# Performance work log

Measured on AMD Instinct MI355X. Metric: run time of the kernel, lower is better.

The kernel has to match this reference:

```python
import jax, jax.numpy as jnp
import numpy as np

DIM, H, MAX_K, RADIUS, KNN_K, ALPHA, LN_EPS = 128, 4, 32, 0.3, 8, 2, 1e-5
DH = DIM // H
SCALE = DH ** -0.5


def _layernorm(x, w, b):
    mu = jnp.mean(x, axis=-1, keepdims=True)
    var = jnp.mean((x - mu) ** 2, axis=-1, keepdims=True)
    return (x - mu) * jax.lax.rsqrt(var + LN_EPS) * w + b


def setup_inputs() -> dict:
    key = jax.random.key(0)
    ks = jax.random.split(key, 12)
    N, M = 50000, 2500
    init = lambda k, shape: (jax.random.normal(k, shape, jnp.float32) * 0.02)
    return {
        "xyz": jax.random.normal(ks[0], (N, 3), jnp.float32),
        "feats": jax.random.normal(ks[1], (N, DIM), jnp.float32),
        "Wq": init(ks[2], (DIM, DIM)),
        "Wk": init(ks[3], (DIM, DIM)),
        "Wv": init(ks[4], (DIM, DIM)),
        "Wo": init(ks[5], (DIM, DIM)),
        "bo": jnp.zeros((DIM,), jnp.float32),
        "n1w": jnp.ones((DIM,), jnp.float32),
        "n1b": jnp.zeros((DIM,), jnp.float32),
        "n2w": jnp.ones((DIM,), jnp.float32),
        "n2b": jnp.zeros((DIM,), jnp.float32),
        "W1": init(ks[6], (DIM, 4 * DIM)),
        "b1": jnp.zeros((4 * DIM,), jnp.float32),
        "W2": init(ks[7], (4 * DIM, DIM)),
        "b2": jnp.zeros((DIM,), jnp.float32),
        "Wp": init(ks[8], (DIM, DIM)),
        "bp": jnp.zeros((DIM,), jnp.float32),
        "idx_center": jax.random.randint(ks[9], (M,), 0, N),
    }


def reference(xyz, feats, Wq, Wk, Wv, Wo, bo, n1w, n1b, n2w, n2b, W1, b1, W2, b2, Wp, bp, idx_center):
    M = idx_center.shape[0]
    center_xyz = xyz[idx_center]          # (M,3)
    center_feat = feats[idx_center]       # (M,C)

    # euclidean distance matrix (M,N) via |a|^2+|b|^2-2ab, safe sqrt (0-grad at 0 like torch.cdist)
    d2 = (jnp.sum(center_xyz ** 2, -1)[:, None] + jnp.sum(xyz ** 2, -1)[None, :]
          - 2.0 * center_xyz @ xyz.T)
    d2 = jnp.maximum(d2, 0.0)
    pos = d2 > 0
    dist = jnp.where(pos, jnp.sqrt(jnp.where(pos, d2, 1.0)), 0.0)  # (M,N)

    # ball query: mask + top-max_k smallest distances
    nbr_mask = dist < RADIUS
    nbr_mask = nbr_mask.at[jnp.arange(M), idx_center].set(True)
    dist_masked = jnp.where(nbr_mask, dist, jnp.inf)
    neg_d, nbr_idx = jax.lax.top_k(-dist_masked, MAX_K)   # (M,K)
    nbr_dist = -neg_d
    mask_valid = jnp.isfinite(nbr_dist)                    # (M,K)

    # gather neighbor feats, zero where invalid
    nbr_feats = jnp.where(mask_valid[..., None], feats[nbr_idx], 0.0)  # (M,K,C)

    # masked local attention per center (tiny heads)
    q = (center_feat @ Wq).reshape(M, H, DH)                       # (M,H,D)
    k = (nbr_feats @ Wk).reshape(M, MAX_K, H, DH).transpose(0, 2, 1, 3)  # (M,H,K,D)
    v = (nbr_feats @ Wv).reshape(M, MAX_K, H, DH).transpose(0, 2, 1, 3)
    attn = jnp.einsum('mhd,mhkd->mhk', q * SCALE, k)
    attn = jnp.where(mask_valid[:, None, :], attn, -1e9)
    attn = jax.nn.softmax(attn, axis=-1)
    out = jnp.einsum('mhk,mhkd->mhd', attn, v)
    # faithful to torch: transpose(1,2) before flatten -> (M, D, H) layout
    out = jnp.swapaxes(out, 1, 2).reshape(M, DIM)
    upd = out @ Wo + bo

    cf = center_feat + _layernorm(upd, n1w, n1b)
    ffn = jax.nn.relu(cf @ W1 + b1) @ W2 + b2
    cf = cf + _layernorm(ffn, n2w, n2b)

    # KNN inverse-distance-weighted upsample back to all N points
    neg_v, knn_idx = jax.lax.top_k(-dist.T, KNN_K)   # (N,k)
    knn_dist = -neg_v
    w = 1.0 / (knn_dist + 1e-6) ** ALPHA
    w = w / jnp.sum(w, axis=-1, keepdims=True)
    out_feats = jnp.einsum('nk,nkc->nc', w, cf[knn_idx])  # (N,C)
    out_feats = out_feats + jax.nn.relu(out_feats @ Wp + bp)
    return feats + out_feats
```

## Files before the change

kernel.cpp:

```cpp
#include <hip/hip_runtime.h>
#include <hip/hip_bf16.h>
#include <stdint.h>

#define DIM    128
#define KMAX   32
#define LN_EPS 1e-5f
#define ATT_SCALE 0.17677669529663687f
#define CAND   2048
#define WTOT   214400
#define PB     32
#define NSTR2  72
#define KSTR   132

typedef unsigned long long u64;
static __device__ __forceinline__ float bf2f(__hip_bfloat16 x) { return __bfloat162float(x); }

static __device__ __forceinline__ float norm32(float x, float y, float z) {
    return __fadd_rn(__fadd_rn(__fmul_rn(x, x), __fmul_rn(y, y)), __fmul_rn(z, z));
}
static __device__ __forceinline__ float d2_32(float cx, float cy, float cz, float cw,
                                              float px, float py, float pz, float pw) {
    float dot = __fmaf_rn(cz, pz, __fmaf_rn(cy, py, __fmul_rn(cx, px)));
    return __fsub_rn(__fadd_rn(cw, pw), __fmul_rn(2.0f, dot));
}
static __device__ __forceinline__ float d2_to_dist(float d2) {
    d2 = fmaxf(d2, 0.0f);
    return (d2 > 0.0f) ? __fsqrt_rn(d2) : 0.0f;
}
static __device__ __forceinline__ float dist32(float cx, float cy, float cz, float cw,
                                               float px, float py, float pz, float pw) {
    return d2_to_dist(d2_32(cx, cy, cz, cw, px, py, pz, pw));
}

static __device__ __forceinline__ float ldf(const void* p, int f32, size_t i) {
    return f32 ? ((const float*)p)[i] : bf2f(((const __hip_bfloat16*)p)[i]);
}
static __device__ __forceinline__ int ldidx(const void* p, int i64, int m) {
    return i64 ? ((const int*)p)[2 * m] : ((const int*)p)[m];
}

struct Ptrs { const void* p[18]; int sz[18]; };

__global__ void probe_dtypes(Ptrs P, int* __restrict__ fl) {
    int j = threadIdx.x;
    if (j >= 18) return;
    const void* x = P.p[j];
    int sz = P.sz[j];
    int flag = 0;
    if (j == 17) {
        const int* ip = (const int*)x;
        int odd_zero = 1, even_nz = 0;
        for (int k = 0; k < 8 && 2 * k + 1 < sz * 2; ++k) {
            if (ip[2 * k + 1] != 0) odd_zero = 0;
            if (ip[2 * k] != 0) even_nz = 1;
        }
        flag = (odd_zero && even_nz) ? 1 : 0;
    } else {
        const __hip_bfloat16* hp = (const __hip_bfloat16*)x;
        int n = sz < 256 ? sz : 256;
        for (int i = 0; i < n; ++i) {
            float w = bf2f(hp[i]);
            if (w != w || fabsf(w) > 1000.0f) { flag = 1; break; }
        }
        if ((j == 7 || j == 9) && bf2f(hp[0]) == 0.0f) flag = 1;
    }
    fl[j] = flag;
}

__global__ __launch_bounds__(256) void conv_prep(Ptrs P, const int* __restrict__ fl,
                                                 float* __restrict__ Wf,
                                                 float4* __restrict__ pnt4,
                                                 float4* __restrict__ cent4,
                                                 int N, int M, int convB) {
    int b = blockIdx.x;
    if (b < convB) {
        int i = b * 256 + threadIdx.x;
        if (i >= WTOT) return;
        int j, off;
        if      (i < 16384)  { j = 2;  off = i; }
        else if (i < 32768)  { j = 3;  off = i - 16384; }
        else if (i < 49152)  { j = 4;  off = i - 32768; }
        else if (i < 65536)  { j = 5;  off = i - 49152; }
        else if (i < 131072) { j = 11; off = i - 65536; }
        else if (i < 196608) { j = 13; off = i - 131072; }
        else if (i < 212992) { j = 15; off = i - 196608; }
        else if (i < 213120) { j = 6;  off = i - 212992; }
        else if (i < 213248) { j = 7;  off = i - 213120; }
        else if (i < 213376) { j = 8;  off = i - 213248; }
        else if (i < 213504) { j = 9;  off = i - 213376; }
        else if (i < 213632) { j = 10; off = i - 213504; }
        else if (i < 214144) { j = 12; off = i - 213632; }
        else if (i < 214272) { j = 14; off = i - 214144; }
        else                 { j = 16; off = i - 214272; }
        Wf[i] = ldf(P.p[j], fl[j], off);
    } else {
        int i = (b - convB) * 256 + threadIdx.x;
        int f0 = fl[0];
        if (i < N) {
            float x = ldf(P.p[0], f0, 3 * i + 0);
            float y = ldf(P.p[0], f0, 3 * i + 1);
            float z = ldf(P.p[0], f0, 3 * i + 2);
            pnt4[i] = make_float4(x, y, z, norm32(x, y, z));
        }
        if (i < M) {
            int c = ldidx(P.p[17], fl[17], i);
            c = (c >= 0 && c < N) ? c : 0;
            float x = ldf(P.p[0], f0, 3 * c + 0);
            float y = ldf(P.p[0], f0, 3 * c + 1);
            float z = ldf(P.p[0], f0, 3 * c + 2);
            cent4[i] = make_float4(x, y, z, norm32(x, y, z));
        }
    }
}

__global__ __launch_bounds__(256) void ball_scan(
    const float4* __restrict__ pnt4,
    const float4* __restrict__ cent4,
    int N, int M, int* __restrict__ nbr_g) {

    __shared__ u64 key[2][CAND];
    __shared__ int s_cnt[2], s_ni[2][KMAX];

    int tid = threadIdx.x;
    int m0 = blockIdx.x * 2, m1 = m0 + 1;
    bool has1 = (m1 < M);
    float4 c0 = cent4[m0];
    float4 c1 = has1 ? cent4[m1] : make_float4(1e30f, 1e30f, 1e30f, 1e30f);

    if (tid < 2) s_cnt[tid] = 0;
    if (tid < KMAX) { s_ni[0][tid] = -1; s_ni[1][tid] = -1; }
    __syncthreads();

    for (int i = tid; i < N; i += 256) {
        float4 p = pnt4[i];
        float d20 = d2_32(c0.x, c0.y, c0.z, c0.w, p.x, p.y, p.z, p.w);
        if (d20 < 0.0901f) {
            float dist = d2_to_dist(d20);
            if (dist < 0.3f) {
                int pos = atomicAdd(&s_cnt[0], 1);
                if (pos < CAND)
                    key[0][pos] = ((u64)__float_as_uint(dist) << 32) | (unsigned)i;
            }
        }
        float d21 = d2_32(c1.x, c1.y, c1.z, c1.w, p.x, p.y, p.z, p.w);
        if (d21 < 0.0901f) {
            float dist = d2_to_dist(d21);
            if (dist < 0.3f) {
                int pos = atomicAdd(&s_cnt[1], 1);
                if (pos < CAND)
                    key[1][pos] = ((u64)__float_as_uint(dist) << 32) | (unsigned)i;
            }
        }
    }
    __syncthreads();

    int half = tid >> 7, t2 = tid & 127;
    int cnth = min(s_cnt[half], CAND);
    if (half == 1 && !has1) cnth = 0;
    for (int i = t2; i < cnth; i += 128) {
        u64 ki = key[half][i];
        int r = 0;
        for (int j = 0; j < cnth; ++j) r += (key[half][j] < ki) ? 1 : 0;
        if (r < KMAX) s_ni[half][r] = (int)(unsigned)(ki & 0xFFFFFFFFULL);
    }
    __syncthreads();
    if (tid < KMAX) nbr_g[m0 * KMAX + tid] = s_ni[0][tid];
    if (has1 && tid >= 128 && tid < 128 + KMAX)
        nbr_g[m1 * KMAX + (tid - 128)] = s_ni[1][tid - 128];
}

#define NFT2(cc, kk) R[(cc) * NSTR2 + (kk)]
#define SKV2(kk, col) R[(kk) * KSTR + (col)]

__global__ __launch_bounds__(256, 4) void attn_ffn(
    const int* __restrict__ nbr_g,
    const void* __restrict__ feats,
    const void* __restrict__ idxc,
    const int* __restrict__ fl,
    const float* __restrict__ Wf,
    float* __restrict__ cf_out, int N, int M) {

    const float* Wqf = Wf;
    const float* Wkf = Wf + 16384;
    const float* Wvf = Wf + 32768;
    const float* Wof = Wf + 49152;
    const float* W1f = Wf + 65536;
    const float* W2f = Wf + 131072;
    const float* Pf  = Wf + 212992;

    __shared__ __align__(16) float R[128 * NSTR2];
    __shared__ int   s_ni[2 * KMAX];
    __shared__ __align__(16) float s_cf[256], s_x[256];
    __shared__ float s_red[8];

    int tid = threadIdx.x;
    int lane = tid & 63, wv = tid >> 6;
    int center = tid >> 7, col = tid & 127;
    int m0 = blockIdx.x * 2;
    int f1 = fl[1], fi = fl[17];

    if (tid < 64) {
        int m2 = m0 + (tid >> 5);
        s_ni[tid] = (m2 < M) ? nbr_g[m2 * KMAX + (tid & 31)] : -1;
    }
    {
        int m2 = m0 + center; m2 = (m2 < M) ? m2 : (M - 1);
        int c = ldidx(idxc, fi, m2);
        c = (c >= 0 && c < N) ? c : 0;
        s_cf[tid] = ldf(feats, f1, (size_t)c * DIM + col);
    }
    __syncthreads();
    for (int t = tid; t < 64 * DIM; t += 256) {
        int kk2 = t >> 7, cc = t & 127;
        int idx = s_ni[kk2];
        float v = (idx >= 0 && idx < N) ? ldf(feats, f1, (size_t)idx * DIM + cc) : 0.0f;
        NFT2(cc, kk2) = v;
    }
    __syncthreads();

    int kq = tid >> 5, cq = tid & 31;
    int k0 = kq * 8, c0 = cq * 4;
    float ka[8][4], va[8][4];
#pragma unroll
    for (int j = 0; j < 8; ++j)
#pragma unroll
        for (int cc2 = 0; cc2 < 4; ++cc2) { ka[j][cc2] = 0.0f; va[j][cc2] = 0.0f; }

#pragma unroll 2
    for (int i = 0; i < DIM; ++i) {
        float4 n0  = *(const float4*)&NFT2(i, k0);
        float4 n1  = *(const float4*)&NFT2(i, k0 + 4);
        float4 wk  = *(const float4*)&Wkf[i * DIM + c0];
        float4 wv4 = *(const float4*)&Wvf[i * DIM + c0];
        float nn[8] = {n0.x, n0.y, n0.z, n0.w, n1.x, n1.y, n1.z, n1.w};
#pragma unroll
        for (int j = 0; j < 8; ++j) {
            float nj = nn[j];
            ka[j][0] = fmaf(nj, wk.x, ka[j][0]);
            ka[j][1] = fmaf(nj, wk.y, ka[j][1]);
            ka[j][2] = fmaf(nj, wk.z, ka[j][2]);
            ka[j][3] = fmaf(nj, wk.w, ka[j][3]);
            va[j][0] = fmaf(nj, wv4.x, va[j][0]);
            va[j][1] = fmaf(nj, wv4.y, va[j][1]);
            va[j][2] = fmaf(nj, wv4.z, va[j][2]);
            va[j][3] = fmaf(nj, wv4.w, va[j][3]);
        }
    }
    __syncthreads();

    float* s_q    = R + 8448;
    float* s_attn = R + 8704;
    float* s_ao   = R + 8960;

#pragma unroll
    for (int j = 0; j < 8; ++j)
        *(float4*)&SKV2(k0 + j, c0) = make_float4(ka[j][0], ka[j][1], ka[j][2], ka[j][3]);
    {
        float acc = 0.0f;
        const float* cfc = s_cf + center * 128;
#pragma unroll 4
        for (int i = 0; i < DIM; i += 4) {
            float4 a = *(const float4*)&cfc[i];
            acc = fmaf(a.x, Wqf[(i + 0) * DIM + col], acc);
            acc = fmaf(a.y, Wqf[(i + 1) * DIM + col], acc);
            acc = fmaf(a.z, Wqf[(i + 2) * DIM + col], acc);
            acc = fmaf(a.w, Wqf[(i + 3) * DIM + col], acc);
        }
        s_q[tid] = acc;
    }
    __syncthreads();

    {
        int h = (tid >> 5) & 3, kk = tid & 31;
        float s = 0.0f;
#pragma unroll
        for (int d = 0; d < 32; ++d)
            s = fmaf(s_q[center * 128 + h * 32 + d], SKV2(center * 32 + kk, h * 32 + d), s);
        s *= ATT_SCALE;
        if (s_ni[center * 32 + kk] < 0) s = -1e9f;
        float mx = s;
        for (int off = 16; off; off >>= 1) mx = fmaxf(mx, __shfl_xor(mx, off, 32));
        float e = expf(s - mx);
        float sm = e;
        for (int off = 16; off; off >>= 1) sm += __shfl_xor(sm, off, 32);
        sm = (sm > 0.0f) ? sm : 1.0f;
        s_attn[tid] = e / sm;
    }
    __syncthreads();
#pragma unroll
    for (int j = 0; j < 8; ++j)
        *(float4*)&SKV2(k0 + j, c0) = make_float4(va[j][0], va[j][1], va[j][2], va[j][3]);
    __syncthreads();

    {
        int h = (tid >> 5) & 3, d = tid & 31;
        float o = 0.0f;
#pragma unroll
        for (int kk = 0; kk < KMAX; ++kk)
            o = fmaf(s_attn[center * 128 + h * 32 + kk], SKV2(center * 32 + kk, h * 32 + d), o);
        s_ao[center * 128 + d * 4 + h] = o;
    }
    __syncthreads();

    float upd = Pf[0 + col];
    {
#pragma unroll 4
        for (int i = 0; i < DIM; i += 4) {
            float4 a = *(const float4*)&s_ao[center * 128 + i];
            upd = fmaf(a.x, Wof[(i + 0) * DIM + col], upd);
            upd = fmaf(a.y, Wof[(i + 1) * DIM + col], upd);
            upd = fmaf(a.z, Wof[(i + 2) * DIM + col], upd);
            upd = fmaf(a.w, Wof[(i + 3) * DIM + col], upd);
        }
        float sum = upd;
        for (int off = 32; off; off >>= 1) sum += __shfl_xor(sum, off, 64);
        if (lane == 0) s_red[wv] = sum;
    }
    __syncthreads();
    float mu = (s_red[center * 2] + s_red[center * 2 + 1]) * (1.0f / 128.0f);
    float xc = upd - mu;
    {
        float q2 = xc * xc;
        for (int off = 32; off; off >>= 1) q2 += __shfl_xor(q2, off, 64);
        if (lane == 0) s_red[4 + wv] = q2;
    }
    __syncthreads();
    float var = (s_red[4 + center * 2] + s_red[5 + center * 2]) * (1.0f / 128.0f);
    float cf1;
    {
        float rs = 1.0f / sqrtf(var + LN_EPS);
        float ln1 = fmaf(xc * rs, Pf[128 + col], Pf[256 + col]);
        cf1 = s_cf[tid] + ln1;
        s_x[tid] = cf1;
    }
    __syncthreads();

    float* s_h = R;
#pragma unroll
    for (int jj = 0; jj < 4; ++jj) {
        int j = col + 128 * jj;
        float a = Pf[640 + j];
#pragma unroll 4
        for (int i = 0; i < DIM; i += 4) {
            float4 v = *(const float4*)&s_x[center * 128 + i];
            a = fmaf(v.x, W1f[(i + 0) * 512 + j], a);
            a = fmaf(v.y, W1f[(i + 1) * 512 + j], a);
            a = fmaf(v.z, W1f[(i + 2) * 512 + j], a);
            a = fmaf(v.w, W1f[(i + 3) * 512 + j], a);
        }
        s_h[center * 512 + j] = fmaxf(a, 0.0f);
    }
    __syncthreads();

    float fa = Pf[1152 + col];
    {
        const float* hc = s_h + center * 512;
#pragma unroll 4
        for (int i = 0; i < 256; i += 4) {
            float4 v = *(const float4*)&hc[i];
            fa = fmaf(v.x, W2f[(i + 0) * DIM + col], fa);
            fa = fmaf(v.y, W2f[(i + 1) * DIM + col], fa);
            fa = fmaf(v.z, W2f[(i + 2) * DIM + col], fa);
            fa = fmaf(v.w, W2f[(i + 3) * DIM + col], fa);
        }
    }
    float fb = 0.0f;
    {
        const float* hc = s_h + center * 512;
#pragma unroll 4
        for (int i = 256; i < 512; i += 4) {
            float4 v = *(const float4*)&hc[i];
            fb = fmaf(v.x, W2f[(i + 0) * DIM + col], fb);
            fb = fmaf(v.y, W2f[(i + 1) * DIM + col], fb);
            fb = fmaf(v.z, W2f[(i + 2) * DIM + col], fb);
            fb = fmaf(v.w, W2f[(i + 3) * DIM + col], fb);
        }
    }
    float ffn = fa + fb;
    {
        float sum = ffn;
        for (int off = 32; off; off >>= 1) sum += __shfl_xor(sum, off, 64);
        if (lane == 0) s_red[wv] = sum;
    }
    __syncthreads();
    mu = (s_red[center * 2] + s_red[center * 2 + 1]) * (1.0f / 128.0f);
    xc = ffn - mu;
    {
        float q2 = xc * xc;
        for (int off = 32; off; off >>= 1) q2 += __shfl_xor(q2, off, 64);
        if (lane == 0) s_red[4 + wv] = q2;
    }
    __syncthreads();
    var = (s_red[4 + center * 2] + s_red[5 + center * 2]) * (1.0f / 128.0f);
    {
        float rs2 = 1.0f / sqrtf(var + LN_EPS);
        float ln2 = fmaf(xc * rs2, Pf[384 + col], Pf[512 + col]);
        int m2 = m0 + center;
        if (m2 < M) cf_out[(size_t)m2 * DIM + col] = cf1 + ln2;
    }
}

#define CSWAP(a, b) { if ((b) < (a)) { u64 t_ = (a); (a) = (b); (b) = t_; } }

static __device__ __forceinline__ float bound8(float vmn) {
    float v = vmn;
    v = fminf(v, __shfl_xor(v, 1, 64));
    v = fminf(v, __shfl_xor(v, 2, 64));
    v = fminf(v, __shfl_xor(v, 4, 64));
    v = fmaxf(v, __shfl_xor(v, 8, 64));
    v = fmaxf(v, __shfl_xor(v, 16, 64));
    v = fmaxf(v, __shfl_xor(v, 32, 64));
    return fmaxf(v, 0.0f) * 1.0000019073486328f;
}

__global__ __launch_bounds__(256) void knn_select(
    const float4* __restrict__ pnt4,
    const float4* __restrict__ cent4,
    const float* __restrict__ cf,
    float* __restrict__ upg,
    int N, int M) {

    __shared__ u64 s_buf[4][4][64];
    __shared__ u64 s_srt[4][4][8];
    __shared__ int s_cnt[4][4];

    int tid = threadIdx.x;
    int lane = tid & 63, wv = tid >> 6;
    int p0 = blockIdx.x * 16 + wv * 4;

    float4 pp[4];
    bool own[4];
#pragma unroll
    for (int e = 0; e < 4; ++e) {
        int p = p0 + e;
        own[e] = (p < N);
        pp[e] = own[e] ? pnt4[p] : make_float4(0.f, 0.f, 0.f, 0.f);
    }

    if (lane < 4) s_cnt[wv][lane] = 0;
    __syncthreads();

    float vmn[4] = {3.4e38f, 3.4e38f, 3.4e38f, 3.4e38f};
    for (int j = lane; j < M; j += 64) {
        float4 cc = cent4[j];
#pragma unroll
        for (int e = 0; e < 4; ++e)
            vmn[e] = fminf(vmn[e], d2_32(cc.x, cc.y, cc.z, cc.w,
                                         pp[e].x, pp[e].y, pp[e].z, pp[e].w));
    }
    float T[4];
#pragma unroll
    for (int e = 0; e < 4; ++e) T[e] = bound8(vmn[e]);

    for (int j = lane; j < M; j += 64) {
        float4 cc = cent4[j];
#pragma unroll
        for (int e = 0; e < 4; ++e) {
            float d2 = d2_32(cc.x, cc.y, cc.z, cc.w,
                             pp[e].x, pp[e].y, pp[e].z, pp[e].w);
            if (d2 <= T[e]) {
                float dist = d2_to_dist(d2);
                u64 key = ((u64)__float_as_uint(dist) << 32) | (unsigned)j;
                int pos = atomicAdd(&s_cnt[wv][e], 1);
                if (pos < 64) s_buf[wv][e][pos] = key;
            }
        }
    }

    int c0 = lane, c1 = lane + 64;
#pragma unroll
    for (int e = 0; e < 4; ++e) {
        int cnt = s_cnt[wv][e];
        if (cnt <= 64 && M >= 8) {
            u64 myk = (lane < cnt) ? s_buf[wv][e][lane] : ~0ULL;
            int r = 0;
            for (int i = 0; i < cnt; ++i) {
                u64 o = s_buf[wv][e][i];
                r += (o < myk) ? 1 : 0;
            }
            if (lane < cnt && r < 8) s_srt[wv][e][r] = myk;
        } else {
            float4 pq = pp[e];
            u64 f0 = ~0ULL, f1_ = ~0ULL, f2_ = ~0ULL, f3 = ~0ULL,
                f4 = ~0ULL, f5 = ~0ULL, f6 = ~0ULL, f7 = ~0ULL;
            for (int j = lane; j < M; j += 64) {
                float4 cc = cent4[j];
                float dist = dist32(cc.x, cc.y, cc.z, cc.w, pq.x, pq.y, pq.z, pq.w);
                u64 key = ((u64)__float_as_uint(dist) << 32) | (unsigned)j;
                if (key < f7) {
                    f7 = key;
                    CSWAP(f6, f7); CSWAP(f5, f6); CSWAP(f4, f5); CSWAP(f3, f4);
                    CSWAP(f2_, f3); CSWAP(f1_, f2_); CSWAP(f0, f1_);
                }
            }
            int ptr2 = 0;
            u64 cur2 = f0;
#pragma unroll
            for (int e2 = 0; e2 < 8; ++e2) {
                u64 v = cur2;
                for (int off = 32; off; off >>= 1) {
                    u64 o = __shfl_down(v, off, 64);
                    v = (o < v) ? o : v;
                }
                u64 gm = __shfl(v, 0, 64);
                if (lane == 0) s_srt[wv][e][e2] = gm;
                if (cur2 == gm) {
                    ptr2++;
                    cur2 = (ptr2 == 1) ? f1_ : (ptr2 == 2) ? f2_ : (ptr2 == 3) ? f3 :
                           (ptr2 == 4) ? f4 : (ptr2 == 5) ? f5 : (ptr2 == 6) ? f6 :
                           (ptr2 == 7) ? f7 : ~0ULL;
                }
            }
        }
        int   ki[8];
        float w8[8];
        float ws = 0.0f;
#pragma unroll
        for (int e2 = 0; e2 < 8; ++e2) {
            u64 gm = s_srt[wv][e][e2];
            float d = __uint_as_float((unsigned)(gm >> 32));
            int ci = (int)(unsigned)(gm & 0xFFFFFFFFULL);
            ci = (ci >= 0 && ci < M) ? ci : 0;
            float t = __fadd_rn(d, 1e-6f);
            float w = 1.0f / __fmul_rn(t, t);
            ws += w;
            ki[e2] = ci;
            w8[e2] = w;
        }
        float inv = 1.0f / ws;
#pragma unroll
        for (int k = 0; k < 8; ++k) w8[k] *= inv;

        float u0 = 0.0f, u1 = 0.0f;
#pragma unroll
        for (int k = 0; k < 8; ++k) {
            const float* row = cf + (size_t)ki[k] * DIM;
            u0 = fmaf(w8[k], row[c0], u0);
            u1 = fmaf(w8[k], row[c1], u1);
        }
        if (own[e]) {
            upg[(size_t)(p0 + e) * DIM + c0] = u0;
            upg[(size_t)(p0 + e) * DIM + c1] = u1;
        }
    }
}

__global__ __launch_bounds__(256) void wp_out(
    const float* __restrict__ Wf,
    const void* __restrict__ feats,
    const int* __restrict__ fl,
    float* __restrict__ out,
    int N) {

    const float* Wpf = Wf + 196608;
    const float* bpf = Wf + 212992 + 1280;

    __shared__ __align__(16) float s_up[PB][132];

    int tid = threadIdx.x;
    int p0 = blockIdx.x * PB;

    for (int f = tid; f < PB * 32; f += 256) {
        int p = f >> 5, i4 = (f & 31) << 2;
        float4 v = make_float4(0.f, 0.f, 0.f, 0.f);
        if (p0 + p < N) v = *(const float4*)&out[(size_t)(p0 + p) * DIM + i4];
        *(float4*)&s_up[p][i4] = v;
    }
    __syncthreads();

    int cq = tid & 31, pq = tid >> 5;
    int c0 = cq << 2;
    int pA = pq << 2;

    float a00 = 0.f, a01 = 0.f, a02 = 0.f, a03 = 0.f;
    float a10 = 0.f, a11 = 0.f, a12 = 0.f, a13 = 0.f;
    float a20 = 0.f, a21 = 0.f, a22 = 0.f, a23 = 0.f;
    float a30 = 0.f, a31 = 0.f, a32 = 0.f, a33 = 0.f;

#pragma unroll 4
    for (int i = 0; i < DIM; ++i) {
        float4 w = *(const float4*)&Wpf[(size_t)i * DIM + c0];
        float u0 = s_up[pA + 0][i];
        float u1 = s_up[pA + 1][i];
        float u2 = s_up[pA + 2][i];
        float u3 = s_up[pA + 3][i];
        a00 = fmaf(u0, w.x, a00); a01 = fmaf(u0, w.y, a01);
        a02 = fmaf(u0, w.z, a02); a03 = fmaf(u0, w.w, a03);
        a10 = fmaf(u1, w.x, a10); a11 = fmaf(u1, w.y, a11);
        a12 = fmaf(u1, w.z, a12); a13 = fmaf(u1, w.w, a13);
        a20 = fmaf(u2, w.x, a20); a21 = fmaf(u2, w.y, a21);
        a22 = fmaf(u2, w.z, a22); a23 = fmaf(u2, w.w, a23);
        a30 = fmaf(u3, w.x, a30); a31 = fmaf(u3, w.y, a31);
        a32 = fmaf(u3, w.z, a32); a33 = fmaf(u3, w.w, a33);
    }

    int f1v = fl[1];
    float4 bp4 = make_float4(bpf[c0 + 0], bpf[c0 + 1], bpf[c0 + 2], bpf[c0 + 3]);

    float accs[4][4] = {{a00, a01, a02, a03}, {a10, a11, a12, a13},
                        {a20, a21, a22, a23}, {a30, a31, a32, a33}};
#pragma unroll
    for (int a = 0; a < 4; ++a) {
        int p = p0 + pA + a;
        if (p < N) {
            float4 u = *(const float4*)&s_up[pA + a][c0];
            float4 o;
            o.x = ldf(feats, f1v, (size_t)p * DIM + c0 + 0) + u.x + fmaxf(bp4.x + accs[a][0], 0.0f);
            o.y = ldf(feats, f1v, (size_t)p * DIM + c0 + 1) + u.y + fmaxf(bp4.y + accs[a][1], 0.0f);
            o.z = ldf(feats, f1v, (size_t)p * DIM + c0 + 2) + u.z + fmaxf(bp4.z + accs[a][2], 0.0f);
            o.w = ldf(feats, f1v, (size_t)p * DIM + c0 + 3) + u.w + fmaxf(bp4.w + accs[a][3], 0.0f);
            *(float4*)&out[(size_t)p * DIM + c0] = o;
        }
    }
}

extern "C" void kernel_launch(void* const* d_in, const int* in_sizes, int n_in,
                              void* d_out, int out_size, void* d_ws, size_t ws_size,
                              hipStream_t stream) {
    int N = in_sizes[0] / 3;
    int M = in_sizes[17];

    Ptrs P;
    for (int j = 0; j < 18; ++j) { P.p[j] = d_in[j]; P.sz[j] = in_sizes[j]; }

    size_t off = 0;
    auto alloc = [&](size_t bytes) -> void* {
        off = (off + 255) & ~(size_t)255;
        void* p = (void*)((char*)d_ws + off);
        off += bytes;
        return p;
    };
    int*    fl    = (int*)alloc(32 * 4);
    float*  Wf    = (float*)alloc((size_t)WTOT * 4);
    float4* pnt4  = (float4*)alloc((size_t)N * 16);
    float4* cent4 = (float4*)alloc((size_t)M * 16);
    float*  cfbuf = (float*)alloc((size_t)M * DIM * 4);
    int*    nbr   = (int*)alloc((size_t)M * KMAX * 4);

    int convB = (WTOT + 255) / 256;
    int NM = (N > M) ? N : M;
    int prepB = (NM + 255) / 256;

    probe_dtypes<<<1, 32, 0, stream>>>(P, fl);
    conv_prep<<<convB + prepB, 256, 0, stream>>>(P, fl, Wf, pnt4, cent4, N, M, convB);
    ball_scan<<<(M + 1) / 2, 256, 0, stream>>>(pnt4, cent4, N, M, nbr);
    attn_ffn<<<(M + 1) / 2, 256, 0, stream>>>(nbr, d_in[1], d_in[17], fl, Wf, cfbuf, N, M);
    knn_select<<<(N + 15) / 16, 256, 0, stream>>>(pnt4, cent4, cfbuf, (float*)d_out, N, M);
    wp_out<<<(N + PB - 1) / PB, 256, 0, stream>>>(Wf, d_in[1], fl, (float*)d_out, N);
}
```

Before: 524.9 us.

## Split attention and FFN into separate kernels with register-resident K/V

The fused attention+FFN kernel is split in two. attn_core runs 512 threads, gathers neighbour features in two 64-channel chunks to cut shared memory, and keeps K/V in registers, computing QK with shuffles and PV with partial sums. It writes only cf1. A new ffn_ln kernel processes four centers per block, so each W1/W2 load is reused across several centers, then applies LN2. This trades an extra launch and a global round-trip of cf for more occupancy and better weight reuse.

```diff
diff --git a/kernel.cpp b/kernel.cpp
--- a/kernel.cpp
+++ b/kernel.cpp
@@ -9,8 +9,8 @@
 #define CAND   2048
 #define WTOT   214400
 #define PB     32
-#define NSTR2  72
-#define KSTR   132
+#define CH     64
+#define GSTR   68
 
 typedef unsigned long long u64;
 static __device__ __forceinline__ float bf2f(__hip_bfloat16 x) { return __bfloat162float(x); }
@@ -169,10 +169,7 @@
         nbr_g[m1 * KMAX + (tid - 128)] = s_ni[1][tid - 128];
 }
 
-#define NFT2(cc, kk) R[(cc) * NSTR2 + (kk)]
-#define SKV2(kk, col) R[(kk) * KSTR + (col)]
-
-__global__ __launch_bounds__(256, 4) void attn_ffn(
+__global__ __launch_bounds__(512, 6) void attn_core(
     const int* __restrict__ nbr_g,
     const void* __restrict__ feats,
     const void* __restrict__ idxc,
@@ -184,18 +181,16 @@
     const float* Wkf = Wf + 16384;
     const float* Wvf = Wf + 32768;
     const float* Wof = Wf + 49152;
-    const float* W1f = Wf + 65536;
-    const float* W2f = Wf + 131072;
     const float* Pf  = Wf + 212992;
 
-    __shared__ __align__(16) float R[128 * NSTR2];
+    __shared__ __align__(16) float G[CH * GSTR];
+    __shared__ __align__(16) float s_pv[16][128];
     __shared__ int   s_ni[2 * KMAX];
-    __shared__ __align__(16) float s_cf[256], s_x[256];
+    __shared__ __align__(16) float s_cf[256], s_q[256], s_attn[256], s_ao[256];
     __shared__ float s_red[8];
 
     int tid = threadIdx.x;
     int lane = tid & 63, wv = tid >> 6;
-    int center = tid >> 7, col = tid & 127;
     int m0 = blockIdx.x * 2;
     int f1 = fl[1], fi = fl[17];
 
@@ -203,59 +198,17 @@
         int m2 = m0 + (tid >> 5);
         s_ni[tid] = (m2 < M) ? nbr_g[m2 * KMAX + (tid & 31)] : -1;
     }
-    {
+    if (tid < 256) {
+        int center = tid >> 7, col = tid & 127;
         int m2 = m0 + center; m2 = (m2 < M) ? m2 : (M - 1);
         int c = ldidx(idxc, fi, m2);
         c = (c >= 0 && c < N) ? c : 0;
         s_cf[tid] = ldf(feats, f1, (size_t)c * DIM + col);
     }
     __syncthreads();
-    for (int t = tid; t < 64 * DIM; t += 256) {
-        int kk2 = t >> 7, cc = t & 127;
-        int idx = s_ni[kk2];
-        float v = (idx >= 0 && idx < N) ? ldf(feats, f1, (size_t)idx * DIM + cc) : 0.0f;
-        NFT2(cc, kk2) = v;
-    }
-    __syncthreads();
-
-    int kq = tid >> 5, cq = tid & 31;
-    int k0 = kq * 8, c0 = cq * 4;
-    float ka[8][4], va[8][4];
-#pragma unroll
-    for (int j = 0; j < 8; ++j)
-#pragma unroll
-        for (int cc2 = 0; cc2 < 4; ++cc2) { ka[j][cc2] = 0.0f; va[j][cc2] = 0.0f; }
-
-#pragma unroll 2
-    for (int i = 0; i < DIM; ++i) {
-        float4 n0  = *(const float4*)&NFT2(i, k0);
-        float4 n1  = *(const float4*)&NFT2(i, k0 + 4);
-        float4 wk  = *(const float4*)&Wkf[i * DIM + c0];
-        float4 wv4 = *(const float4*)&Wvf[i * DIM + c0];
-        float nn[8] = {n0.x, n0.y, n0.z, n0.w, n1.x, n1.y, n1.z, n1.w};
-#pragma unroll
-        for (int j = 0; j < 8; ++j) {
-            float nj = nn[j];
-            ka[j][0] = fmaf(nj, wk.x, ka[j][0]);
-            ka[j][1] = fmaf(nj, wk.y, ka[j][1]);
-            ka[j][2] = fmaf(nj, wk.z, ka[j][2]);
-            ka[j][3] = fmaf(nj, wk.w, ka[j][3]);
-            va[j][0] = fmaf(nj, wv4.x, va[j][0]);
-            va[j][1] = fmaf(nj, wv4.y, va[j][1]);
-            va[j][2] = fmaf(nj, wv4.z, va[j][2]);
-            va[j][3] = fmaf(nj, wv4.w, va[j][3]);
-        }
-    }
-    __syncthreads();
-
-    float* s_q    = R + 8448;
-    float* s_attn = R + 8704;
-    float* s_ao   = R + 8960;
-
-#pragma unroll
-    for (int j = 0; j < 8; ++j)
-        *(float4*)&SKV2(k0 + j, c0) = make_float4(ka[j][0], ka[j][1], ka[j][2], ka[j][3]);
-    {
+
+    if (tid < 256) {
+        int center = tid >> 7, col = tid & 127;
         float acc = 0.0f;
         const float* cfc = s_cf + center * 128;
 #pragma unroll 4
@@ -268,15 +221,77 @@
         }
         s_q[tid] = acc;
     }
-    __syncthreads();
+
+    int kq = tid >> 5;
+    int cq = tid & 31;
+    int k0 = kq * 4, c0 = cq * 4;
+    int cent = kq >> 3;
+    float ka[4][4], va[4][4];
+#pragma unroll
+    for (int j = 0; j < 4; ++j)
+#pragma unroll
+        for (int t = 0; t < 4; ++t) { ka[j][t] = 0.0f; va[j][t] = 0.0f; }
+
+    for (int r = 0; r < 2; ++r) {
+        if (r) __syncthreads();
+        for (int t = tid; t < 64 * CH; t += 512) {
+            int kk = t >> 6, cc = t & 63;
+            int idx = s_ni[kk];
+            float v = (idx >= 0 && idx < N)
+                    ? ldf(feats, f1, (size_t)idx * DIM + r * CH + cc) : 0.0f;
+            G[cc * GSTR + kk] = v;
+        }
+        __syncthreads();
+#pragma unroll 2
+        for (int i = 0; i < CH; ++i) {
+            float4 n = *(const float4*)&G[i * GSTR + k0];
+            int gi = r * CH + i;
+            float4 wk  = *(const float4*)&Wkf[gi * DIM + c0];
+            float4 wv4 = *(const float4*)&Wvf[gi * DIM + c0];
+            float nn[4] = {n.x, n.y, n.z, n.w};
+#pragma unroll
+            for (int j = 0; j < 4; ++j) {
+                float nj = nn[j];
+                ka[j][0] = fmaf(nj, wk.x, ka[j][0]);
+                ka[j][1] = fmaf(nj, wk.y, ka[j][1]);
+                ka[j][2] = fmaf(nj, wk.z, ka[j][2]);
+                ka[j][3] = fmaf(nj, wk.w, ka[j][3]);
+                va[j][0] = fmaf(nj, wv4.x, va[j][0]);
+                va[j][1] = fmaf(nj, wv4.y, va[j][1]);
+                va[j][2] = fmaf(nj, wv4.z, va[j][2]);
+                va[j][3] = fmaf(nj, wv4.w, va[j][3]);
+            }
+        }
+    }
 
     {
-        int h = (tid >> 5) & 3, kk = tid & 31;
-        float s = 0.0f;
-#pragma unroll
-        for (int d = 0; d < 32; ++d)
-            s = fmaf(s_q[center * 128 + h * 32 + d], SKV2(center * 32 + kk, h * 32 + d), s);
-        s *= ATT_SCALE;
+        const float* qc = s_q + cent * 128;
+        float part[4];
+#pragma unroll
+        for (int j = 0; j < 4; ++j) {
+            float p = 0.0f;
+            p = fmaf(qc[c0 + 0], ka[j][0], p);
+            p = fmaf(qc[c0 + 1], ka[j][1], p);
+            p = fmaf(qc[c0 + 2], ka[j][2], p);
+            p = fmaf(qc[c0 + 3], ka[j][3], p);
+            p += __shfl_xor(p, 1, 64);
+            p += __shfl_xor(p, 2, 64);
+            p += __shfl_xor(p, 4, 64);
+            part[j] = p;
+        }
+        if ((cq & 7) == 0) {
+            int h = cq >> 3;
+#pragma unroll
+            for (int j = 0; j < 4; ++j)
+                s_attn[cent * 128 + h * 32 + (kq & 7) * 4 + j] = part[j];
+        }
+    }
+    __syncthreads();
+
+    if (tid < 256) {
+        int center = tid >> 7;
+        int kk = tid & 31;
+        float s = s_attn[tid] * ATT_SCALE;
         if (s_ni[center * 32 + kk] < 0) s = -1e9f;
         float mx = s;
         for (int off = 16; off; off >>= 1) mx = fmaxf(mx, __shfl_xor(mx, off, 32));
@@ -287,23 +302,40 @@
         s_attn[tid] = e / sm;
     }
     __syncthreads();
-#pragma unroll
-    for (int j = 0; j < 8; ++j)
-        *(float4*)&SKV2(k0 + j, c0) = make_float4(va[j][0], va[j][1], va[j][2], va[j][3]);
-    __syncthreads();
 
     {
-        int h = (tid >> 5) & 3, d = tid & 31;
-        float o = 0.0f;
-#pragma unroll
-        for (int kk = 0; kk < KMAX; ++kk)
-            o = fmaf(s_attn[center * 128 + h * 32 + kk], SKV2(center * 32 + kk, h * 32 + d), o);
-        s_ao[center * 128 + d * 4 + h] = o;
-    }
-    __syncthreads();
-
-    float upd = Pf[0 + col];
-    {
+        int h = cq >> 3;
+        float pvp0 = 0.0f, pvp1 = 0.0f, pvp2 = 0.0f, pvp3 = 0.0f;
+#pragma unroll
+        for (int j = 0; j < 4; ++j) {
+            float a = s_attn[cent * 128 + h * 32 + (kq & 7) * 4 + j];
+            pvp0 = fmaf(a, va[j][0], pvp0);
+            pvp1 = fmaf(a, va[j][1], pvp1);
+            pvp2 = fmaf(a, va[j][2], pvp2);
+            pvp3 = fmaf(a, va[j][3], pvp3);
+        }
+        *(float4*)&s_pv[kq][c0] = make_float4(pvp0, pvp1, pvp2, pvp3);
+    }
+    __syncthreads();
+
+    if (tid < 256) {
+        int cb = tid >> 7, cc2 = tid & 127;
+        float o = s_pv[cb * 8 + 0][cc2];
+        o += s_pv[cb * 8 + 1][cc2];
+        o += s_pv[cb * 8 + 2][cc2];
+        o += s_pv[cb * 8 + 3][cc2];
+        o += s_pv[cb * 8 + 4][cc2];
+        o += s_pv[cb * 8 + 5][cc2];
+        o += s_pv[cb * 8 + 6][cc2];
+        o += s_pv[cb * 8 + 7][cc2];
+        s_ao[cb * 128 + (cc2 & 31) * 4 + (cc2 >> 5)] = o;
+    }
+    __syncthreads();
+
+    float upd = 0.0f, xc = 0.0f;
+    int center = tid >> 7, col = tid & 127;
+    if (tid < 256) {
+        upd = Pf[0 + col];
 #pragma unroll 4
         for (int i = 0; i < DIM; i += 4) {
             float4 a = *(const float4*)&s_ao[center * 128 + i];
@@ -317,86 +349,128 @@
         if (lane == 0) s_red[wv] = sum;
     }
     __syncthreads();
-    float mu = (s_red[center * 2] + s_red[center * 2 + 1]) * (1.0f / 128.0f);
-    float xc = upd - mu;
-    {
+    if (tid < 256) {
+        float mu = (s_red[center * 2] + s_red[center * 2 + 1]) * (1.0f / 128.0f);
+        xc = upd - mu;
         float q2 = xc * xc;
         for (int off = 32; off; off >>= 1) q2 += __shfl_xor(q2, off, 64);
         if (lane == 0) s_red[4 + wv] = q2;
     }
     __syncthreads();
-    float var = (s_red[4 + center * 2] + s_red[5 + center * 2]) * (1.0f / 128.0f);
-    float cf1;
-    {
+    if (tid < 256) {
+        float var = (s_red[4 + center * 2] + s_red[5 + center * 2]) * (1.0f / 128.0f);
         float rs = 1.0f / sqrtf(var + LN_EPS);
         float ln1 = fmaf(xc * rs, Pf[128 + col], Pf[256 + col]);
-        cf1 = s_cf[tid] + ln1;
-        s_x[tid] = cf1;
-    }
-    __syncthreads();
-
-    float* s_h = R;
-#pragma unroll
-    for (int jj = 0; jj < 4; ++jj) {
-        int j = col + 128 * jj;
-        float a = Pf[640 + j];
-#pragma unroll 4
-        for (int i = 0; i < DIM; i += 4) {
-            float4 v = *(const float4*)&s_x[center * 128 + i];
-            a = fmaf(v.x, W1f[(i + 0) * 512 + j], a);
-            a = fmaf(v.y, W1f[(i + 1) * 512 + j], a);
-            a = fmaf(v.z, W1f[(i + 2) * 512 + j], a);
-            a = fmaf(v.w, W1f[(i + 3) * 512 + j], a);
-        }
-        s_h[center * 512 + j] = fmaxf(a, 0.0f);
-    }
-    __syncthreads();
-
-    float fa = Pf[1152 + col];
+        float cf1 = s_cf[tid] + ln1;
+        int m2 = m0 + center;
+        if (m2 < M) cf_out[(size_t)m2 * DIM + col] = cf1;
+    }
+}
+
+__global__ __launch_bounds__(256) void ffn_ln(
+    const float* __restrict__ Wf,
+    float* __restrict__ cf, int M) {
+
+    const float* W1f = Wf + 65536;
+    const float* W2f = Wf + 131072;
+    const float* Pf  = Wf + 212992;
+
+    __shared__ __align__(16) float s_x[512];
+    __shared__ __align__(16) float s_h[2048];
+    __shared__ float s_p2[2][4][128];
+    __shared__ float s_red[8];
+
+    int tid = threadIdx.x, lane = tid & 63, wv = tid >> 6;
+    int m0 = blockIdx.x * 4;
+
+    for (int t = tid; t < 512; t += 256) {
+        int cent = t >> 7, c = t & 127;
+        int m = m0 + cent;
+        s_x[t] = (m < M) ? cf[(size_t)m * DIM + c] : 0.0f;
+    }
+    __syncthreads();
+
     {
-        const float* hc = s_h + center * 512;
-#pragma unroll 4
-        for (int i = 0; i < 256; i += 4) {
-            float4 v = *(const float4*)&hc[i];
-            fa = fmaf(v.x, W2f[(i + 0) * DIM + col], fa);
-            fa = fmaf(v.y, W2f[(i + 1) * DIM + col], fa);
-            fa = fmaf(v.z, W2f[(i + 2) * DIM + col], fa);
-            fa = fmaf(v.w, W2f[(i + 3) * DIM + col], fa);
-        }
-    }
-    float fb = 0.0f;
+        int pairh = tid >> 7;
+        int j0 = (tid & 127) * 4;
+        float4 b1q = *(const float4*)&Pf[640 + j0];
+        float aA0 = b1q.x, aA1 = b1q.y, aA2 = b1q.z, aA3 = b1q.w;
+        float aB0 = b1q.x, aB1 = b1q.y, aB2 = b1q.z, aB3 = b1q.w;
+        const float* xA = s_x + (2 * pairh) * 128;
+        const float* xB = s_x + (2 * pairh + 1) * 128;
+#pragma unroll 2
+        for (int i4 = 0; i4 < 32; ++i4) {
+            float4 xa = *(const float4*)&xA[i4 * 4];
+            float4 xb = *(const float4*)&xB[i4 * 4];
+#pragma unroll
+            for (int s = 0; s < 4; ++s) {
+                float4 w = *(const float4*)&W1f[(i4 * 4 + s) * 512 + j0];
+                float va_ = (&xa.x)[s], vb_ = (&xb.x)[s];
+                aA0 = fmaf(va_, w.x, aA0); aA1 = fmaf(va_, w.y, aA1);
+                aA2 = fmaf(va_, w.z, aA2); aA3 = fmaf(va_, w.w, aA3);
+                aB0 = fmaf(vb_, w.x, aB0); aB1 = fmaf(vb_, w.y, aB1);
+                aB2 = fmaf(vb_, w.z, aB2); aB3 = fmaf(vb_, w.w, aB3);
+            }
+        }
+        *(float4*)&s_h[(2 * pairh) * 512 + j0] =
+            make_float4(fmaxf(aA0, 0.0f), fmaxf(aA1, 0.0f), fmaxf(aA2, 0.0f), fmaxf(aA3, 0.0f));
+        *(float4*)&s_h[(2 * pairh + 1) * 512 + j0] =
+            make_float4(fmaxf(aB0, 0.0f), fmaxf(aB1, 0.0f), fmaxf(aB2, 0.0f), fmaxf(aB3, 0.0f));
+    }
+    __syncthreads();
+
     {
-        const float* hc = s_h + center * 512;
-#pragma unroll 4
-        for (int i = 256; i < 512; i += 4) {
-            float4 v = *(const float4*)&hc[i];
-            fb = fmaf(v.x, W2f[(i + 0) * DIM + col], fb);
-            fb = fmaf(v.y, W2f[(i + 1) * DIM + col], fb);
-            fb = fmaf(v.z, W2f[(i + 2) * DIM + col], fb);
-            fb = fmaf(v.w, W2f[(i + 3) * DIM + col], fb);
-        }
-    }
-    float ffn = fa + fb;
-    {
+        int kh = tid >> 7;
+        int c = tid & 127;
+        float acc0 = (kh == 0) ? Pf[1152 + c] : 0.0f;
+        float acc1 = acc0, acc2 = acc0, acc3 = acc0;
+        const float* h0 = s_h + 0 * 512 + kh * 256;
+        const float* h1 = s_h + 1 * 512 + kh * 256;
+        const float* h2 = s_h + 2 * 512 + kh * 256;
+        const float* h3 = s_h + 3 * 512 + kh * 256;
+#pragma unroll 2
+        for (int i4 = 0; i4 < 64; ++i4) {
+            float4 q0 = *(const float4*)&h0[i4 * 4];
+            float4 q1 = *(const float4*)&h1[i4 * 4];
+            float4 q2 = *(const float4*)&h2[i4 * 4];
+            float4 q3 = *(const float4*)&h3[i4 * 4];
+#pragma unroll
+            for (int s = 0; s < 4; ++s) {
+                float w = W2f[(kh * 256 + i4 * 4 + s) * DIM + c];
+                acc0 = fmaf((&q0.x)[s], w, acc0);
+                acc1 = fmaf((&q1.x)[s], w, acc1);
+                acc2 = fmaf((&q2.x)[s], w, acc2);
+                acc3 = fmaf((&q3.x)[s], w, acc3);
+            }
+        }
+        s_p2[kh][0][c] = acc0;
+        s_p2[kh][1][c] = acc1;
+        s_p2[kh][2][c] = acc2;
+        s_p2[kh][3][c] = acc3;
+    }
+    __syncthreads();
+
+    for (int rr = 0; rr < 2; ++rr) {
+        int cl = tid >> 7;
+        int cent = rr * 2 + cl;
+        int c = tid & 127;
+        float ffn = s_p2[0][cent][c] + s_p2[1][cent][c];
         float sum = ffn;
         for (int off = 32; off; off >>= 1) sum += __shfl_xor(sum, off, 64);
         if (lane == 0) s_red[wv] = sum;
-    }
-    __syncthreads();
-    mu = (s_red[center * 2] + s_red[center * 2 + 1]) * (1.0f / 128.0f);
-    xc = ffn - mu;
-    {
+        __syncthreads();
+        float mu = (s_red[cl * 2] + s_red[cl * 2 + 1]) * (1.0f / 128.0f);
+        float xc = ffn - mu;
         float q2 = xc * xc;
         for (int off = 32; off; off >>= 1) q2 += __shfl_xor(q2, off, 64);
         if (lane == 0) s_red[4 + wv] = q2;
-    }
-    __syncthreads();
-    var = (s_red[4 + center * 2] + s_red[5 + center * 2]) * (1.0f / 128.0f);
-    {
+        __syncthreads();
+        float var = (s_red[4 + cl * 2] + s_red[5 + cl * 2]) * (1.0f / 128.0f);
         float rs2 = 1.0f / sqrtf(var + LN_EPS);
-        float ln2 = fmaf(xc * rs2, Pf[384 + col], Pf[512 + col]);
-        int m2 = m0 + center;
-        if (m2 < M) cf_out[(size_t)m2 * DIM + col] = cf1 + ln2;
+        float ln2 = fmaf(xc * rs2, Pf[384 + c], Pf[512 + c]);
+        int m = m0 + cent;
+        if (m < M) cf[(size_t)m * DIM + c] = s_x[cent * 128 + c] + ln2;
+        __syncthreads();
     }
 }
 
@@ -644,7 +718,8 @@
     probe_dtypes<<<1, 32, 0, stream>>>(P, fl);
     conv_prep<<<convB + prepB, 256, 0, stream>>>(P, fl, Wf, pnt4, cent4, N, M, convB);
     ball_scan<<<(M + 1) / 2, 256, 0, stream>>>(pnt4, cent4, N, M, nbr);
-    attn_ffn<<<(M + 1) / 2, 256, 0, stream>>>(nbr, d_in[1], d_in[17], fl, Wf, cfbuf, N, M);
+    attn_core<<<(M + 1) / 2, 512, 0, stream>>>(nbr, d_in[1], d_in[17], fl, Wf, cfbuf, N, M);
+    ffn_ln<<<(M + 3) / 4, 256, 0, stream>>>(Wf, cfbuf, M);
     knn_select<<<(N + 15) / 16, 256, 0, stream>>>(pnt4, cent4, cfbuf, (float*)d_out, N, M);
     wp_out<<<(N + PB - 1) / PB, 256, 0, stream>>>(Wf, d_in[1], fl, (float*)d_out, N);
 }
```

Measured after the change: 527.8 us. No clear change (+0.6%).
